# Optimization experiments

Hardware: AMD Instinct MI355X
Metric: run time of the kernel (lower is better)

The kernel has to match this reference:

```python
import jax, jax.numpy as jnp
import numpy as np

D_MODEL = 512
NHEAD = 8


def setup_inputs() -> dict:
    key = jax.random.key(0)
    k0, k1, k2 = jax.random.split(key, 3)
    s = 1.0 / np.sqrt(D_MODEL)  # torch default uniform init bound (xavier-ish)
    return {
        "x": jax.random.normal(k0, (2, 4096, D_MODEL), dtype=jnp.float32),
        "in_proj_w": jax.random.uniform(k1, (3 * D_MODEL, D_MODEL), jnp.float32, -s, s),
        "in_proj_b": jnp.zeros((3 * D_MODEL,), jnp.float32),
        "out_proj_w": jax.random.uniform(k2, (D_MODEL, D_MODEL), jnp.float32, -s, s),
        "out_proj_b": jnp.zeros((D_MODEL,), jnp.float32),
        "window_size": 128,
    }


def reference(x, in_proj_w, in_proj_b, out_proj_w, out_proj_b, window_size):
    # Faithful to nn.MultiheadAttention (eval mode, dropout inactive).
    # NOTE: PyTorch bool attn_mask: True = disallowed. The module sets True
    # INSIDE the window, so in-window positions are masked OUT.
    B, S, D = x.shape
    H = NHEAD
    hd = D // H

    qkv = x @ in_proj_w.T + in_proj_b                      # [B,S,3D]
    q, k, v = jnp.split(qkv, 3, axis=-1)
    q = q.reshape(B, S, H, hd).transpose(0, 2, 1, 3)       # [B,H,S,hd]
    k = k.reshape(B, S, H, hd).transpose(0, 2, 1, 3)
    v = v.reshape(B, S, H, hd).transpose(0, 2, 1, 3)

    scores = jnp.einsum('bhqd,bhkd->bhqk', q, k) / jnp.sqrt(jnp.float32(hd))

    idx = jnp.arange(S)
    in_window = jnp.abs(idx[:, None] - idx[None, :]) <= window_size  # [S,S]
    scores = jnp.where(in_window, -jnp.inf, scores)

    attn = jax.nn.softmax(scores, axis=-1)                 # [B,H,S,S]
    ctx = jnp.einsum('bhqk,bhkd->bhqd', attn, v)           # [B,H,S,hd]
    ctx = ctx.transpose(0, 2, 1, 3).reshape(B, S, D)       # [B,S,D]
    return ctx @ out_proj_w.T + out_proj_b
```

## Files before the change

kernel.cpp:

```cpp
#include <hip/hip_runtime.h>
#include <hip/hip_bf16.h>

typedef unsigned short u16;
typedef __bf16 bf16x8 __attribute__((ext_vector_type(8)));
typedef float f32x4 __attribute__((ext_vector_type(4)));

__device__ __forceinline__ f32x4 mfma16(bf16x8 a, bf16x8 b, f32x4 c) {
    return __builtin_amdgcn_mfma_f32_16x16x32_bf16(a, b, c, 0, 0, 0);
}

__device__ __forceinline__ u16 f2b(float x) {
    union { float f; unsigned u; } a; a.f = x;
    unsigned r = a.u + 0x7fffu + ((a.u >> 16) & 1u);
    return (u16)(r >> 16);
}

__global__ __launch_bounds__(256) void k_cast(const float* __restrict__ src,
                                              u16* __restrict__ dst, int n) {
    int i = (blockIdx.x * 256 + threadIdx.x) * 4;
    if (i >= n) return;
    float4 f = *(const float4*)&src[i];
    u16 o[4] = { f2b(f.x), f2b(f.y), f2b(f.z), f2b(f.w) };
    *(uint2*)&dst[i] = *(uint2*)o;
}

__global__ __launch_bounds__(256) void k_gemm_qkv(const u16* __restrict__ xb,
                                                  const u16* __restrict__ wb,
                                                  const float* __restrict__ bias,
                                                  u16* __restrict__ qkvout) {
    __shared__ u16 As[128][40];
    __shared__ u16 Ws[64][40];
    const int tid = threadIdx.x;
    const int w = tid >> 6, lane = tid & 63, l15 = lane & 15, quad = lane >> 4;
    const int mb = blockIdx.x * 128, nb = blockIdx.y * 64;

    f32x4 acc[2][4];
#pragma unroll
    for (int i = 0; i < 2; i++)
#pragma unroll
        for (int j = 0; j < 4; j++) acc[i][j] = (f32x4){0.f, 0.f, 0.f, 0.f};

    for (int k0 = 0; k0 < 512; k0 += 32) {
        {
            int row = tid >> 1, cc = (tid & 1) * 16;
            const u16* g = &xb[(size_t)(mb + row) * 512 + k0 + cc];
            *(uint4*)&As[row][cc]     = *(const uint4*)g;
            *(uint4*)&As[row][cc + 8] = *(const uint4*)(g + 8);
            int wrow = tid >> 2, wcc = (tid & 3) * 8;
            *(uint4*)&Ws[wrow][wcc] = *(const uint4*)&wb[(size_t)(nb + wrow) * 512 + k0 + wcc];
        }
        __syncthreads();
        bf16x8 a0 = *(const bf16x8*)&As[w * 32 + l15][quad * 8];
        bf16x8 a1 = *(const bf16x8*)&As[w * 32 + 16 + l15][quad * 8];
#pragma unroll
        for (int nt = 0; nt < 4; nt++) {
            bf16x8 bfr = *(const bf16x8*)&Ws[nt * 16 + l15][quad * 8];
            acc[0][nt] = mfma16(a0, bfr, acc[0][nt]);
            acc[1][nt] = mfma16(a1, bfr, acc[1][nt]);
        }
        __syncthreads();
    }
    const int seg = nb >> 9;
    const int hh  = (nb >> 6) & 7;
    u16* obase = qkvout + (size_t)seg * (16ull * 4096 * 64);
    if (seg < 2) {
        const float sc = (seg == 0) ? 0.125f * 1.44269504088896340736f : 1.0f;
#pragma unroll
        for (int mt = 0; mt < 2; mt++)
#pragma unroll
            for (int nt = 0; nt < 4; nt++)
#pragma unroll
                for (int r = 0; r < 4; r++) {
                    int m = mb + w * 32 + mt * 16 + quad * 4 + r;
                    int dloc = nt * 16 + l15;
                    float vv = (acc[mt][nt][r] + bias[nb + dloc]) * sc;
                    int b = m >> 12, s = m & 4095;
                    obase[((size_t)((b * 8 + hh) * 4096 + s)) * 64 + dloc] = f2b(vv);
                }
    } else {
#pragma unroll
        for (int mt = 0; mt < 2; mt++)
#pragma unroll
            for (int nt = 0; nt < 4; nt++) {
                int m0 = mb + w * 32 + mt * 16 + quad * 4;
                int b = m0 >> 12, s0 = m0 & 4095;
                int dloc = nt * 16 + l15;
                u16 o[4];
#pragma unroll
                for (int r = 0; r < 4; r++)
                    o[r] = f2b(acc[mt][nt][r] + bias[nb + dloc]);
                *(uint2*)&obase[((size_t)((b * 8 + hh) * 64 + dloc)) * 4096 + s0] = *(uint2*)o;
            }
    }
}

__global__ __launch_bounds__(128) void k_attn(const u16* __restrict__ qkv,
                                              u16* __restrict__ ctx,
                                              const int* __restrict__ win) {
    __shared__ u16 Ks[64][72];
    __shared__ u16 Vt[64][72];
    __shared__ u16 Ps[64][72];
    const int tid = threadIdx.x;
    const int w = tid >> 6, lane = tid & 63, l15 = lane & 15, quad = lane >> 4;
    const int bh = blockIdx.y;
    const int qb0 = blockIdx.x * 64;
    const int W = win[0];
    const u16* qg = qkv;
    const u16* kg = qkv + 16ull * 4096 * 64;
    const u16* vg = qkv + 32ull * 4096 * 64;
    const size_t bhb = (size_t)bh * 4096 * 64;

    bf16x8 qf[2][2];
#pragma unroll
    for (int g = 0; g < 2; g++) {
        const u16* qrow = &qg[bhb + (size_t)(qb0 + w * 32 + g * 16 + l15) * 64];
        qf[g][0] = *(const bf16x8*)&qrow[quad * 8];
        qf[g][1] = *(const bf16x8*)&qrow[32 + quad * 8];
    }

    f32x4 O[2][4];
#pragma unroll
    for (int g = 0; g < 2; g++)
#pragma unroll
        for (int nt = 0; nt < 4; nt++) O[g][nt] = (f32x4){0.f, 0.f, 0.f, 0.f};
    float lsum[2] = {0.f, 0.f};

    const int srow = tid >> 1, shalf = (tid & 1) * 32;
    const u16* kgr = &kg[bhb + (size_t)srow * 64 + shalf];
    const u16* vgr = &vg[((size_t)bh * 64 + srow) * 4096 + shalf];

    for (int kb = 0; kb < 4096; kb += 64) {
        if (max(qb0 + 63 - kb, kb + 63 - qb0) <= W) continue;
        bool partial = (kb + 63 >= qb0 - W) && (kb <= qb0 + 63 + W);
        {
            const u16* kp = kgr + (size_t)kb * 64;
            *(uint4*)&Ks[srow][shalf]      = *(const uint4*)kp;
            *(uint4*)&Ks[srow][shalf + 8]  = *(const uint4*)(kp + 8);
            *(uint4*)&Ks[srow][shalf + 16] = *(const uint4*)(kp + 16);
            *(uint4*)&Ks[srow][shalf + 24] = *(const uint4*)(kp + 24);
            const u16* vp = vgr + kb;
            *(uint4*)&Vt[srow][shalf]      = *(const uint4*)vp;
            *(uint4*)&Vt[srow][shalf + 8]  = *(const uint4*)(vp + 8);
            *(uint4*)&Vt[srow][shalf + 16] = *(const uint4*)(vp + 16);
            *(uint4*)&Vt[srow][shalf + 24] = *(const uint4*)(vp + 24);
        }
        __syncthreads();
        f32x4 C[4][2];
#pragma unroll
        for (int nt = 0; nt < 4; nt++) {
            bf16x8 kf0 = *(const bf16x8*)&Ks[nt * 16 + l15][quad * 8];
            bf16x8 kf1 = *(const bf16x8*)&Ks[nt * 16 + l15][32 + quad * 8];
#pragma unroll
            for (int g = 0; g < 2; g++) {
                f32x4 z = (f32x4){0.f, 0.f, 0.f, 0.f};
                C[nt][g] = mfma16(kf0, qf[g][0], z);
                C[nt][g] = mfma16(kf1, qf[g][1], C[nt][g]);
            }
        }
        if (!partial) {
#pragma unroll
            for (int g = 0; g < 2; g++)
#pragma unroll
                for (int nt = 0; nt < 4; nt++) {
                    u16 o[4];
#pragma unroll
                    for (int r = 0; r < 4; r++) {
                        float p = __builtin_amdgcn_exp2f(C[nt][g][r]);
                        lsum[g] += p;
                        o[r] = f2b(p);
                    }
                    *(uint2*)&Ps[w * 32 + g * 16 + l15][nt * 16 + quad * 4] = *(uint2*)o;
                }
        } else {
#pragma unroll
            for (int g = 0; g < 2; g++) {
                int qr = qb0 + w * 32 + g * 16 + l15;
#pragma unroll
                for (int nt = 0; nt < 4; nt++) {
                    u16 o[4];
#pragma unroll
                    for (int r = 0; r < 4; r++) {
                        int key = kb + nt * 16 + quad * 4 + r;
                        int dd = qr - key; dd = dd < 0 ? -dd : dd;
                        float p = (dd <= W) ? 0.f : __builtin_amdgcn_exp2f(C[nt][g][r]);
                        lsum[g] += p;
                        o[r] = f2b(p);
                    }
                    *(uint2*)&Ps[w * 32 + g * 16 + l15][nt * 16 + quad * 4] = *(uint2*)o;
                }
            }
        }
#pragma unroll
        for (int ks = 0; ks < 2; ks++) {
            bf16x8 pa0 = *(const bf16x8*)&Ps[w * 32 + l15][ks * 32 + quad * 8];
            bf16x8 pa1 = *(const bf16x8*)&Ps[w * 32 + 16 + l15][ks * 32 + quad * 8];
#pragma unroll
            for (int nt = 0; nt < 4; nt++) {
                bf16x8 vb = *(const bf16x8*)&Vt[nt * 16 + l15][ks * 32 + quad * 8];
                O[0][nt] = mfma16(pa0, vb, O[0][nt]);
                O[1][nt] = mfma16(pa1, vb, O[1][nt]);
            }
        }
        __syncthreads();
    }
#pragma unroll
    for (int g = 0; g < 2; g++) {
        lsum[g] += __shfl_xor(lsum[g], 16);
        lsum[g] += __shfl_xor(lsum[g], 32);
    }
    int b = bh >> 3, h = bh & 7;
#pragma unroll
    for (int g = 0; g < 2; g++)
#pragma unroll
        for (int r = 0; r < 4; r++) {
            float inv = 1.0f / __shfl(lsum[g], quad * 4 + r);
            int qr = qb0 + w * 32 + g * 16 + quad * 4 + r;
            size_t rowoff = ((size_t)(b * 4096 + qr)) * 512 + h * 64;
#pragma unroll
            for (int nt = 0; nt < 4; nt++)
                ctx[rowoff + nt * 16 + l15] = f2b(O[g][nt][r] * inv);
        }
}

__global__ __launch_bounds__(256) void k_gemm_out(const u16* __restrict__ ab,
                                                  const u16* __restrict__ wb,
                                                  const float* __restrict__ bias,
                                                  float* __restrict__ out) {
    __shared__ u16 As[128][40];
    __shared__ u16 Ws[64][40];
    const int tid = threadIdx.x;
    const int w = tid >> 6, lane = tid & 63, l15 = lane & 15, quad = lane >> 4;
    const int mb = blockIdx.x * 128, nb = blockIdx.y * 64;

    f32x4 acc[2][4];
#pragma unroll
    for (int i = 0; i < 2; i++)
#pragma unroll
        for (int j = 0; j < 4; j++) acc[i][j] = (f32x4){0.f, 0.f, 0.f, 0.f};

    for (int k0 = 0; k0 < 512; k0 += 32) {
        {
            int row = tid >> 1, cc = (tid & 1) * 16;
            const u16* g = &ab[(size_t)(mb + row) * 512 + k0 + cc];
            *(uint4*)&As[row][cc]     = *(const uint4*)g;
            *(uint4*)&As[row][cc + 8] = *(const uint4*)(g + 8);
            int wrow = tid >> 2, wcc = (tid & 3) * 8;
            *(uint4*)&Ws[wrow][wcc] = *(const uint4*)&wb[(size_t)(nb + wrow) * 512 + k0 + wcc];
        }
        __syncthreads();
        bf16x8 a0 = *(const bf16x8*)&As[w * 32 + l15][quad * 8];
        bf16x8 a1 = *(const bf16x8*)&As[w * 32 + 16 + l15][quad * 8];
#pragma unroll
        for (int nt = 0; nt < 4; nt++) {
            bf16x8 bfr = *(const bf16x8*)&Ws[nt * 16 + l15][quad * 8];
            acc[0][nt] = mfma16(a0, bfr, acc[0][nt]);
            acc[1][nt] = mfma16(a1, bfr, acc[1][nt]);
        }
        __syncthreads();
    }
#pragma unroll
    for (int mt = 0; mt < 2; mt++)
#pragma unroll
        for (int nt = 0; nt < 4; nt++)
#pragma unroll
            for (int r = 0; r < 4; r++) {
                int m = mb + w * 32 + mt * 16 + quad * 4 + r;
                int n = nb + nt * 16 + l15;
                out[(size_t)m * 512 + n] = acc[mt][nt][r] + bias[n];
            }
}

extern "C" void kernel_launch(void* const* d_in, const int* in_sizes, int n_in,
                              void* d_out, int out_size, void* d_ws, size_t ws_size,
                              hipStream_t stream) {
    const float* x    = (const float*)d_in[0];
    const float* wqkv = (const float*)d_in[1];
    const float* bqkv = (const float*)d_in[2];
    const float* wout = (const float*)d_in[3];
    const float* bout = (const float*)d_in[4];
    const int*   win  = (const int*)d_in[5];
    float* out = (float*)d_out;

    u16* xb    = (u16*)d_ws;
    u16* wqkvb = xb    + 8192ull * 512;
    u16* woutb = wqkvb + 1536ull * 512;
    u16* qkvb  = woutb + 512ull * 512;
    u16* ctxb  = qkvb  + 3ull * 16 * 4096 * 64;

    k_cast<<<4096, 256, 0, stream>>>(x, xb, 8192 * 512);
    k_cast<<<768, 256, 0, stream>>>(wqkv, wqkvb, 1536 * 512);
    k_cast<<<256, 256, 0, stream>>>(wout, woutb, 512 * 512);
    k_gemm_qkv<<<dim3(64, 24), 256, 0, stream>>>(xb, wqkvb, bqkv, qkvb);
    k_attn<<<dim3(64, 16), 128, 0, stream>>>(qkvb, ctxb, win);
    k_gemm_out<<<dim3(64, 8), 256, 0, stream>>>(ctxb, woutb, bout, out);
}
```

Before: 239.1 us.

## Fuse fp32-to-bf16 casts into GEMM loads and enlarge attention query tile

```diff
diff --git a/kernel.cpp b/kernel.cpp
--- a/kernel.cpp
+++ b/kernel.cpp
@@ -15,17 +15,8 @@
     return (u16)(r >> 16);
 }
 
-__global__ __launch_bounds__(256) void k_cast(const float* __restrict__ src,
-                                              u16* __restrict__ dst, int n) {
-    int i = (blockIdx.x * 256 + threadIdx.x) * 4;
-    if (i >= n) return;
-    float4 f = *(const float4*)&src[i];
-    u16 o[4] = { f2b(f.x), f2b(f.y), f2b(f.z), f2b(f.w) };
-    *(uint2*)&dst[i] = *(uint2*)o;
-}
-
-__global__ __launch_bounds__(256) void k_gemm_qkv(const u16* __restrict__ xb,
-                                                  const u16* __restrict__ wb,
+__global__ __launch_bounds__(256) void k_gemm_qkv(const float* __restrict__ x,
+                                                  const float* __restrict__ wqkv,
                                                   const float* __restrict__ bias,
                                                   u16* __restrict__ qkvout) {
     __shared__ u16 As[128][40];
@@ -42,12 +33,23 @@
 
     for (int k0 = 0; k0 < 512; k0 += 32) {
         {
-            int row = tid >> 1, cc = (tid & 1) * 16;
-            const u16* g = &xb[(size_t)(mb + row) * 512 + k0 + cc];
-            *(uint4*)&As[row][cc]     = *(const uint4*)g;
-            *(uint4*)&As[row][cc + 8] = *(const uint4*)(g + 8);
-            int wrow = tid >> 2, wcc = (tid & 3) * 8;
-            *(uint4*)&Ws[wrow][wcc] = *(const uint4*)&wb[(size_t)(nb + wrow) * 512 + k0 + wcc];
+            int row = tid >> 1, seg = (tid & 1) * 16;
+            const float* g = &x[(size_t)(mb + row) * 512 + k0 + seg];
+            u16 o[16];
+#pragma unroll
+            for (int e = 0; e < 4; e++) {
+                float4 f = *(const float4*)(g + e * 4);
+                o[e * 4 + 0] = f2b(f.x); o[e * 4 + 1] = f2b(f.y);
+                o[e * 4 + 2] = f2b(f.z); o[e * 4 + 3] = f2b(f.w);
+            }
+            *(uint4*)&As[row][seg]     = *(uint4*)&o[0];
+            *(uint4*)&As[row][seg + 8] = *(uint4*)&o[8];
+            int wrow = tid >> 2, wseg = (tid & 3) * 8;
+            const float* gw = &wqkv[(size_t)(nb + wrow) * 512 + k0 + wseg];
+            float4 h0 = *(const float4*)gw, h1 = *(const float4*)(gw + 4);
+            u16 ow[8] = { f2b(h0.x), f2b(h0.y), f2b(h0.z), f2b(h0.w),
+                          f2b(h1.x), f2b(h1.y), f2b(h1.z), f2b(h1.w) };
+            *(uint4*)&Ws[wrow][wseg] = *(uint4*)ow;
         }
         __syncthreads();
         bf16x8 a0 = *(const bf16x8*)&As[w * 32 + l15][quad * 8];
@@ -99,39 +101,39 @@
                                               const int* __restrict__ win) {
     __shared__ u16 Ks[64][72];
     __shared__ u16 Vt[64][72];
-    __shared__ u16 Ps[64][72];
+    __shared__ u16 Ps[128][72];
     const int tid = threadIdx.x;
     const int w = tid >> 6, lane = tid & 63, l15 = lane & 15, quad = lane >> 4;
     const int bh = blockIdx.y;
-    const int qb0 = blockIdx.x * 64;
+    const int qb0 = blockIdx.x * 128;
     const int W = win[0];
     const u16* qg = qkv;
     const u16* kg = qkv + 16ull * 4096 * 64;
     const u16* vg = qkv + 32ull * 4096 * 64;
     const size_t bhb = (size_t)bh * 4096 * 64;
 
-    bf16x8 qf[2][2];
-#pragma unroll
-    for (int g = 0; g < 2; g++) {
-        const u16* qrow = &qg[bhb + (size_t)(qb0 + w * 32 + g * 16 + l15) * 64];
+    bf16x8 qf[4][2];
+#pragma unroll
+    for (int g = 0; g < 4; g++) {
+        const u16* qrow = &qg[bhb + (size_t)(qb0 + w * 64 + g * 16 + l15) * 64];
         qf[g][0] = *(const bf16x8*)&qrow[quad * 8];
         qf[g][1] = *(const bf16x8*)&qrow[32 + quad * 8];
     }
 
-    f32x4 O[2][4];
-#pragma unroll
-    for (int g = 0; g < 2; g++)
+    f32x4 O[4][4];
+#pragma unroll
+    for (int g = 0; g < 4; g++)
 #pragma unroll
         for (int nt = 0; nt < 4; nt++) O[g][nt] = (f32x4){0.f, 0.f, 0.f, 0.f};
-    float lsum[2] = {0.f, 0.f};
+    float lsum[4] = {0.f, 0.f, 0.f, 0.f};
 
     const int srow = tid >> 1, shalf = (tid & 1) * 32;
     const u16* kgr = &kg[bhb + (size_t)srow * 64 + shalf];
     const u16* vgr = &vg[((size_t)bh * 64 + srow) * 4096 + shalf];
 
     for (int kb = 0; kb < 4096; kb += 64) {
-        if (max(qb0 + 63 - kb, kb + 63 - qb0) <= W) continue;
-        bool partial = (kb + 63 >= qb0 - W) && (kb <= qb0 + 63 + W);
+        if (max(qb0 + 127 - kb, kb + 63 - qb0) <= W) continue;
+        bool partial = (kb + 63 >= qb0 - W) && (kb <= qb0 + 127 + W);
         {
             const u16* kp = kgr + (size_t)kb * 64;
             *(uint4*)&Ks[srow][shalf]      = *(const uint4*)kp;
@@ -145,36 +147,35 @@
             *(uint4*)&Vt[srow][shalf + 24] = *(const uint4*)(vp + 24);
         }
         __syncthreads();
-        f32x4 C[4][2];
+        bf16x8 kf[4][2];
 #pragma unroll
         for (int nt = 0; nt < 4; nt++) {
-            bf16x8 kf0 = *(const bf16x8*)&Ks[nt * 16 + l15][quad * 8];
-            bf16x8 kf1 = *(const bf16x8*)&Ks[nt * 16 + l15][32 + quad * 8];
-#pragma unroll
-            for (int g = 0; g < 2; g++) {
+            kf[nt][0] = *(const bf16x8*)&Ks[nt * 16 + l15][quad * 8];
+            kf[nt][1] = *(const bf16x8*)&Ks[nt * 16 + l15][32 + quad * 8];
+        }
+#pragma unroll
+        for (int g = 0; g < 4; g++) {
+            f32x4 C[4];
+#pragma unroll
+            for (int nt = 0; nt < 4; nt++) {
                 f32x4 z = (f32x4){0.f, 0.f, 0.f, 0.f};
-                C[nt][g] = mfma16(kf0, qf[g][0], z);
-                C[nt][g] = mfma16(kf1, qf[g][1], C[nt][g]);
-            }
-        }
-        if (!partial) {
-#pragma unroll
-            for (int g = 0; g < 2; g++)
+                C[nt] = mfma16(kf[nt][0], qf[g][0], z);
+                C[nt] = mfma16(kf[nt][1], qf[g][1], C[nt]);
+            }
+            if (!partial) {
 #pragma unroll
                 for (int nt = 0; nt < 4; nt++) {
                     u16 o[4];
 #pragma unroll
                     for (int r = 0; r < 4; r++) {
-                        float p = __builtin_amdgcn_exp2f(C[nt][g][r]);
+                        float p = __builtin_amdgcn_exp2f(C[nt][r]);
                         lsum[g] += p;
                         o[r] = f2b(p);
                     }
-                    *(uint2*)&Ps[w * 32 + g * 16 + l15][nt * 16 + quad * 4] = *(uint2*)o;
+                    *(uint2*)&Ps[w * 64 + g * 16 + l15][nt * 16 + quad * 4] = *(uint2*)o;
                 }
-        } else {
-#pragma unroll
-            for (int g = 0; g < 2; g++) {
-                int qr = qb0 + w * 32 + g * 16 + l15;
+            } else {
+                int qr = qb0 + w * 64 + g * 16 + l15;
 #pragma unroll
                 for (int nt = 0; nt < 4; nt++) {
                     u16 o[4];
@@ -182,39 +183,42 @@
                     for (int r = 0; r < 4; r++) {
                         int key = kb + nt * 16 + quad * 4 + r;
                         int dd = qr - key; dd = dd < 0 ? -dd : dd;
-                        float p = (dd <= W) ? 0.f : __builtin_amdgcn_exp2f(C[nt][g][r]);
+                        float p = (dd <= W) ? 0.f : __builtin_amdgcn_exp2f(C[nt][r]);
                         lsum[g] += p;
                         o[r] = f2b(p);
                     }
-                    *(uint2*)&Ps[w * 32 + g * 16 + l15][nt * 16 + quad * 4] = *(uint2*)o;
+                    *(uint2*)&Ps[w * 64 + g * 16 + l15][nt * 16 + quad * 4] = *(uint2*)o;
                 }
             }
         }
 #pragma unroll
         for (int ks = 0; ks < 2; ks++) {
-            bf16x8 pa0 = *(const bf16x8*)&Ps[w * 32 + l15][ks * 32 + quad * 8];
-            bf16x8 pa1 = *(const bf16x8*)&Ps[w * 32 + 16 + l15][ks * 32 + quad * 8];
+            bf16x8 pa[4];
+#pragma unroll
+            for (int g = 0; g < 4; g++)
+                pa[g] = *(const bf16x8*)&Ps[w * 64 + g * 16 + l15][ks * 32 + quad * 8];
 #pragma unroll
             for (int nt = 0; nt < 4; nt++) {
                 bf16x8 vb = *(const bf16x8*)&Vt[nt * 16 + l15][ks * 32 + quad * 8];
-                O[0][nt] = mfma16(pa0, vb, O[0][nt]);
-                O[1][nt] = mfma16(pa1, vb, O[1][nt]);
-            }
-        }
-        __syncthreads();
-    }
-#pragma unroll
-    for (int g = 0; g < 2; g++) {
+#pragma unroll
+                for (int g = 0; g < 4; g++)
+                    O[g][nt] = mfma16(pa[g], vb, O[g][nt]);
+            }
+        }
+        __syncthreads();
+    }
+#pragma unroll
+    for (int g = 0; g < 4; g++) {
         lsum[g] += __shfl_xor(lsum[g], 16);
         lsum[g] += __shfl_xor(lsum[g], 32);
     }
     int b = bh >> 3, h = bh & 7;
 #pragma unroll
-    for (int g = 0; g < 2; g++)
+    for (int g = 0; g < 4; g++)
 #pragma unroll
         for (int r = 0; r < 4; r++) {
             float inv = 1.0f / __shfl(lsum[g], quad * 4 + r);
-            int qr = qb0 + w * 32 + g * 16 + quad * 4 + r;
+            int qr = qb0 + w * 64 + g * 16 + quad * 4 + r;
             size_t rowoff = ((size_t)(b * 4096 + qr)) * 512 + h * 64;
 #pragma unroll
             for (int nt = 0; nt < 4; nt++)
@@ -223,7 +227,7 @@
 }
 
 __global__ __launch_bounds__(256) void k_gemm_out(const u16* __restrict__ ab,
-                                                  const u16* __restrict__ wb,
+                                                  const float* __restrict__ wout,
                                                   const float* __restrict__ bias,
                                                   float* __restrict__ out) {
     __shared__ u16 As[128][40];
@@ -244,8 +248,12 @@
             const u16* g = &ab[(size_t)(mb + row) * 512 + k0 + cc];
             *(uint4*)&As[row][cc]     = *(const uint4*)g;
             *(uint4*)&As[row][cc + 8] = *(const uint4*)(g + 8);
-            int wrow = tid >> 2, wcc = (tid & 3) * 8;
-            *(uint4*)&Ws[wrow][wcc] = *(const uint4*)&wb[(size_t)(nb + wrow) * 512 + k0 + wcc];
+            int wrow = tid >> 2, wseg = (tid & 3) * 8;
+            const float* gw = &wout[(size_t)(nb + wrow) * 512 + k0 + wseg];
+            float4 h0 = *(const float4*)gw, h1 = *(const float4*)(gw + 4);
+            u16 ow[8] = { f2b(h0.x), f2b(h0.y), f2b(h0.z), f2b(h0.w),
+                          f2b(h1.x), f2b(h1.y), f2b(h1.z), f2b(h1.w) };
+            *(uint4*)&Ws[wrow][wseg] = *(uint4*)ow;
         }
         __syncthreads();
         bf16x8 a0 = *(const bf16x8*)&As[w * 32 + l15][quad * 8];
@@ -281,16 +289,10 @@
     const int*   win  = (const int*)d_in[5];
     float* out = (float*)d_out;
 
-    u16* xb    = (u16*)d_ws;
-    u16* wqkvb = xb    + 8192ull * 512;
-    u16* woutb = wqkvb + 1536ull * 512;
-    u16* qkvb  = woutb + 512ull * 512;
-    u16* ctxb  = qkvb  + 3ull * 16 * 4096 * 64;
-
-    k_cast<<<4096, 256, 0, stream>>>(x, xb, 8192 * 512);
-    k_cast<<<768, 256, 0, stream>>>(wqkv, wqkvb, 1536 * 512);
-    k_cast<<<256, 256, 0, stream>>>(wout, woutb, 512 * 512);
-    k_gemm_qkv<<<dim3(64, 24), 256, 0, stream>>>(xb, wqkvb, bqkv, qkvb);
-    k_attn<<<dim3(64, 16), 128, 0, stream>>>(qkvb, ctxb, win);
-    k_gemm_out<<<dim3(64, 8), 256, 0, stream>>>(ctxb, woutb, bout, out);
-}
+    u16* qkvb = (u16*)d_ws;
+    u16* ctxb = qkvb + 3ull * 16 * 4096 * 64;
+
+    k_gemm_qkv<<<dim3(64, 24), 256, 0, stream>>>(x, wqkv, bqkv, qkvb);
+    k_attn<<<dim3(32, 16), 128, 0, stream>>>(qkvb, ctxb, win);
+    k_gemm_out<<<dim3(64, 8), 256, 0, stream>>>(ctxb, wout, bout, out);
+}
```

Measured after the change: 301.0 us. +25.9%, slower.

## Keep attention probabilities in registers and widen GEMM N-tiles to 128

Applied to the files above, without the earlier changes.

```diff
diff --git a/kernel.cpp b/kernel.cpp
--- a/kernel.cpp
+++ b/kernel.cpp
@@ -3,10 +3,14 @@
 
 typedef unsigned short u16;
 typedef __bf16 bf16x8 __attribute__((ext_vector_type(8)));
+typedef short s16x4 __attribute__((ext_vector_type(4)));
 typedef float f32x4 __attribute__((ext_vector_type(4)));
 
 __device__ __forceinline__ f32x4 mfma16(bf16x8 a, bf16x8 b, f32x4 c) {
     return __builtin_amdgcn_mfma_f32_16x16x32_bf16(a, b, c, 0, 0, 0);
+}
+__device__ __forceinline__ f32x4 mfma16k16(s16x4 a, s16x4 b, f32x4 c) {
+    return __builtin_amdgcn_mfma_f32_16x16x16bf16_1k(a, b, c, 0, 0, 0);
 }
 
 __device__ __forceinline__ u16 f2b(float x) {
@@ -29,16 +33,16 @@
                                                   const float* __restrict__ bias,
                                                   u16* __restrict__ qkvout) {
     __shared__ u16 As[128][40];
-    __shared__ u16 Ws[64][40];
+    __shared__ u16 Ws[128][40];
     const int tid = threadIdx.x;
     const int w = tid >> 6, lane = tid & 63, l15 = lane & 15, quad = lane >> 4;
-    const int mb = blockIdx.x * 128, nb = blockIdx.y * 64;
-
-    f32x4 acc[2][4];
+    const int mb = blockIdx.x * 128, nb = blockIdx.y * 128;
+
+    f32x4 acc[2][8];
 #pragma unroll
     for (int i = 0; i < 2; i++)
 #pragma unroll
-        for (int j = 0; j < 4; j++) acc[i][j] = (f32x4){0.f, 0.f, 0.f, 0.f};
+        for (int j = 0; j < 8; j++) acc[i][j] = (f32x4){0.f, 0.f, 0.f, 0.f};
 
     for (int k0 = 0; k0 < 512; k0 += 32) {
         {
@@ -46,14 +50,15 @@
             const u16* g = &xb[(size_t)(mb + row) * 512 + k0 + cc];
             *(uint4*)&As[row][cc]     = *(const uint4*)g;
             *(uint4*)&As[row][cc + 8] = *(const uint4*)(g + 8);
-            int wrow = tid >> 2, wcc = (tid & 3) * 8;
-            *(uint4*)&Ws[wrow][wcc] = *(const uint4*)&wb[(size_t)(nb + wrow) * 512 + k0 + wcc];
+            const u16* gw = &wb[(size_t)(nb + row) * 512 + k0 + cc];
+            *(uint4*)&Ws[row][cc]     = *(const uint4*)gw;
+            *(uint4*)&Ws[row][cc + 8] = *(const uint4*)(gw + 8);
         }
         __syncthreads();
         bf16x8 a0 = *(const bf16x8*)&As[w * 32 + l15][quad * 8];
         bf16x8 a1 = *(const bf16x8*)&As[w * 32 + 16 + l15][quad * 8];
 #pragma unroll
-        for (int nt = 0; nt < 4; nt++) {
+        for (int nt = 0; nt < 8; nt++) {
             bf16x8 bfr = *(const bf16x8*)&Ws[nt * 16 + l15][quad * 8];
             acc[0][nt] = mfma16(a0, bfr, acc[0][nt]);
             acc[1][nt] = mfma16(a1, bfr, acc[1][nt]);
@@ -61,45 +66,47 @@
         __syncthreads();
     }
     const int seg = nb >> 9;
-    const int hh  = (nb >> 6) & 7;
     u16* obase = qkvout + (size_t)seg * (16ull * 4096 * 64);
     if (seg < 2) {
         const float sc = (seg == 0) ? 0.125f * 1.44269504088896340736f : 1.0f;
 #pragma unroll
         for (int mt = 0; mt < 2; mt++)
 #pragma unroll
-            for (int nt = 0; nt < 4; nt++)
+            for (int nt = 0; nt < 8; nt++) {
+                int dcol = nb + nt * 16 + l15;
+                int hh = (dcol >> 6) & 7, dloc = dcol & 63;
+                float bs = bias[dcol];
 #pragma unroll
                 for (int r = 0; r < 4; r++) {
                     int m = mb + w * 32 + mt * 16 + quad * 4 + r;
-                    int dloc = nt * 16 + l15;
-                    float vv = (acc[mt][nt][r] + bias[nb + dloc]) * sc;
+                    float vv = (acc[mt][nt][r] + bs) * sc;
                     int b = m >> 12, s = m & 4095;
                     obase[((size_t)((b * 8 + hh) * 4096 + s)) * 64 + dloc] = f2b(vv);
                 }
+            }
     } else {
 #pragma unroll
         for (int mt = 0; mt < 2; mt++)
 #pragma unroll
-            for (int nt = 0; nt < 4; nt++) {
+            for (int nt = 0; nt < 8; nt++) {
+                int dcol = nb + nt * 16 + l15;
+                int hh = (dcol >> 6) & 7, dloc = dcol & 63;
+                float bs = bias[dcol];
                 int m0 = mb + w * 32 + mt * 16 + quad * 4;
                 int b = m0 >> 12, s0 = m0 & 4095;
-                int dloc = nt * 16 + l15;
                 u16 o[4];
 #pragma unroll
-                for (int r = 0; r < 4; r++)
-                    o[r] = f2b(acc[mt][nt][r] + bias[nb + dloc]);
+                for (int r = 0; r < 4; r++) o[r] = f2b(acc[mt][nt][r] + bs);
                 *(uint2*)&obase[((size_t)((b * 8 + hh) * 64 + dloc)) * 4096 + s0] = *(uint2*)o;
             }
     }
 }
 
-__global__ __launch_bounds__(128) void k_attn(const u16* __restrict__ qkv,
-                                              u16* __restrict__ ctx,
-                                              const int* __restrict__ win) {
+__global__ __launch_bounds__(128, 2) void k_attn(const u16* __restrict__ qkv,
+                                                 u16* __restrict__ ctx,
+                                                 const int* __restrict__ win) {
     __shared__ u16 Ks[64][72];
     __shared__ u16 Vt[64][72];
-    __shared__ u16 Ps[64][72];
     const int tid = threadIdx.x;
     const int w = tid >> 6, lane = tid & 63, l15 = lane & 15, quad = lane >> 4;
     const int bh = blockIdx.y;
@@ -122,7 +129,7 @@
 #pragma unroll
     for (int g = 0; g < 2; g++)
 #pragma unroll
-        for (int nt = 0; nt < 4; nt++) O[g][nt] = (f32x4){0.f, 0.f, 0.f, 0.f};
+        for (int mb = 0; mb < 4; mb++) O[g][mb] = (f32x4){0.f, 0.f, 0.f, 0.f};
     float lsum[2] = {0.f, 0.f};
 
     const int srow = tid >> 1, shalf = (tid & 1) * 32;
@@ -145,61 +152,55 @@
             *(uint4*)&Vt[srow][shalf + 24] = *(const uint4*)(vp + 24);
         }
         __syncthreads();
-        f32x4 C[4][2];
+        bf16x8 kf[4][2];
 #pragma unroll
         for (int nt = 0; nt < 4; nt++) {
-            bf16x8 kf0 = *(const bf16x8*)&Ks[nt * 16 + l15][quad * 8];
-            bf16x8 kf1 = *(const bf16x8*)&Ks[nt * 16 + l15][32 + quad * 8];
-#pragma unroll
-            for (int g = 0; g < 2; g++) {
+            kf[nt][0] = *(const bf16x8*)&Ks[nt * 16 + l15][quad * 8];
+            kf[nt][1] = *(const bf16x8*)&Ks[nt * 16 + l15][32 + quad * 8];
+        }
+        s16x4 vf[4][4];
+#pragma unroll
+        for (int mb = 0; mb < 4; mb++)
+#pragma unroll
+            for (int nt = 0; nt < 4; nt++)
+                vf[mb][nt] = *(const s16x4*)&Vt[mb * 16 + l15][nt * 16 + quad * 4];
+#pragma unroll
+        for (int g = 0; g < 2; g++) {
+            f32x4 C[4];
+#pragma unroll
+            for (int nt = 0; nt < 4; nt++) {
                 f32x4 z = (f32x4){0.f, 0.f, 0.f, 0.f};
-                C[nt][g] = mfma16(kf0, qf[g][0], z);
-                C[nt][g] = mfma16(kf1, qf[g][1], C[nt][g]);
-            }
-        }
-        if (!partial) {
-#pragma unroll
-            for (int g = 0; g < 2; g++)
-#pragma unroll
-                for (int nt = 0; nt < 4; nt++) {
-                    u16 o[4];
+                C[nt] = mfma16(kf[nt][0], qf[g][0], z);
+                C[nt] = mfma16(kf[nt][1], qf[g][1], C[nt]);
+            }
+            s16x4 pb[4];
+            if (!partial) {
+#pragma unroll
+                for (int nt = 0; nt < 4; nt++)
 #pragma unroll
                     for (int r = 0; r < 4; r++) {
-                        float p = __builtin_amdgcn_exp2f(C[nt][g][r]);
+                        float p = __builtin_amdgcn_exp2f(C[nt][r]);
                         lsum[g] += p;
-                        o[r] = f2b(p);
+                        pb[nt][r] = (short)f2b(p);
                     }
-                    *(uint2*)&Ps[w * 32 + g * 16 + l15][nt * 16 + quad * 4] = *(uint2*)o;
-                }
-        } else {
-#pragma unroll
-            for (int g = 0; g < 2; g++) {
+            } else {
                 int qr = qb0 + w * 32 + g * 16 + l15;
 #pragma unroll
-                for (int nt = 0; nt < 4; nt++) {
-                    u16 o[4];
+                for (int nt = 0; nt < 4; nt++)
 #pragma unroll
                     for (int r = 0; r < 4; r++) {
                         int key = kb + nt * 16 + quad * 4 + r;
                         int dd = qr - key; dd = dd < 0 ? -dd : dd;
-                        float p = (dd <= W) ? 0.f : __builtin_amdgcn_exp2f(C[nt][g][r]);
+                        float p = (dd <= W) ? 0.f : __builtin_amdgcn_exp2f(C[nt][r]);
                         lsum[g] += p;
-                        o[r] = f2b(p);
+                        pb[nt][r] = (short)f2b(p);
                     }
-                    *(uint2*)&Ps[w * 32 + g * 16 + l15][nt * 16 + quad * 4] = *(uint2*)o;
-                }
-            }
-        }
-#pragma unroll
-        for (int ks = 0; ks < 2; ks++) {
-            bf16x8 pa0 = *(const bf16x8*)&Ps[w * 32 + l15][ks * 32 + quad * 8];
-            bf16x8 pa1 = *(const bf16x8*)&Ps[w * 32 + 16 + l15][ks * 32 + quad * 8];
-#pragma unroll
-            for (int nt = 0; nt < 4; nt++) {
-                bf16x8 vb = *(const bf16x8*)&Vt[nt * 16 + l15][ks * 32 + quad * 8];
-                O[0][nt] = mfma16(pa0, vb, O[0][nt]);
-                O[1][nt] = mfma16(pa1, vb, O[1][nt]);
-            }
+            }
+#pragma unroll
+            for (int nt = 0; nt < 4; nt++)
+#pragma unroll
+                for (int mb = 0; mb < 4; mb++)
+                    O[g][mb] = mfma16k16(vf[mb][nt], pb[nt], O[g][mb]);
         }
         __syncthreads();
     }
@@ -210,16 +211,18 @@
     }
     int b = bh >> 3, h = bh & 7;
 #pragma unroll
-    for (int g = 0; g < 2; g++)
-#pragma unroll
-        for (int r = 0; r < 4; r++) {
-            float inv = 1.0f / __shfl(lsum[g], quad * 4 + r);
-            int qr = qb0 + w * 32 + g * 16 + quad * 4 + r;
-            size_t rowoff = ((size_t)(b * 4096 + qr)) * 512 + h * 64;
-#pragma unroll
-            for (int nt = 0; nt < 4; nt++)
-                ctx[rowoff + nt * 16 + l15] = f2b(O[g][nt][r] * inv);
-        }
+    for (int g = 0; g < 2; g++) {
+        float inv = 1.0f / lsum[g];
+        int qr = qb0 + w * 32 + g * 16 + l15;
+        size_t rowoff = ((size_t)(b * 4096 + qr)) * 512 + h * 64;
+#pragma unroll
+        for (int mb = 0; mb < 4; mb++) {
+            u16 o[4];
+#pragma unroll
+            for (int r = 0; r < 4; r++) o[r] = f2b(O[g][mb][r] * inv);
+            *(uint2*)&ctx[rowoff + mb * 16 + quad * 4] = *(uint2*)o;
+        }
+    }
 }
 
 __global__ __launch_bounds__(256) void k_gemm_out(const u16* __restrict__ ab,
@@ -227,16 +230,16 @@
                                                   const float* __restrict__ bias,
                                                   float* __restrict__ out) {
     __shared__ u16 As[128][40];
-    __shared__ u16 Ws[64][40];
+    __shared__ u16 Ws[128][40];
     const int tid = threadIdx.x;
     const int w = tid >> 6, lane = tid & 63, l15 = lane & 15, quad = lane >> 4;
-    const int mb = blockIdx.x * 128, nb = blockIdx.y * 64;
-
-    f32x4 acc[2][4];
+    const int mb = blockIdx.x * 128, nb = blockIdx.y * 128;
+
+    f32x4 acc[2][8];
 #pragma unroll
     for (int i = 0; i < 2; i++)
 #pragma unroll
-        for (int j = 0; j < 4; j++) acc[i][j] = (f32x4){0.f, 0.f, 0.f, 0.f};
+        for (int j = 0; j < 8; j++) acc[i][j] = (f32x4){0.f, 0.f, 0.f, 0.f};
 
     for (int k0 = 0; k0 < 512; k0 += 32) {
         {
@@ -244,14 +247,15 @@
             const u16* g = &ab[(size_t)(mb + row) * 512 + k0 + cc];
             *(uint4*)&As[row][cc]     = *(const uint4*)g;
             *(uint4*)&As[row][cc + 8] = *(const uint4*)(g + 8);
-            int wrow = tid >> 2, wcc = (tid & 3) * 8;
-            *(uint4*)&Ws[wrow][wcc] = *(const uint4*)&wb[(size_t)(nb + wrow) * 512 + k0 + wcc];
+            const u16* gw = &wb[(size_t)(nb + row) * 512 + k0 + cc];
+            *(uint4*)&Ws[row][cc]     = *(const uint4*)gw;
+            *(uint4*)&Ws[row][cc + 8] = *(const uint4*)(gw + 8);
         }
         __syncthreads();
         bf16x8 a0 = *(const bf16x8*)&As[w * 32 + l15][quad * 8];
         bf16x8 a1 = *(const bf16x8*)&As[w * 32 + 16 + l15][quad * 8];
 #pragma unroll
-        for (int nt = 0; nt < 4; nt++) {
+        for (int nt = 0; nt < 8; nt++) {
             bf16x8 bfr = *(const bf16x8*)&Ws[nt * 16 + l15][quad * 8];
             acc[0][nt] = mfma16(a0, bfr, acc[0][nt]);
             acc[1][nt] = mfma16(a1, bfr, acc[1][nt]);
@@ -261,13 +265,15 @@
 #pragma unroll
     for (int mt = 0; mt < 2; mt++)
 #pragma unroll
-        for (int nt = 0; nt < 4; nt++)
+        for (int nt = 0; nt < 8; nt++) {
+            int n = nb + nt * 16 + l15;
+            float bs = bias[n];
 #pragma unroll
             for (int r = 0; r < 4; r++) {
                 int m = mb + w * 32 + mt * 16 + quad * 4 + r;
-                int n = nb + nt * 16 + l15;
-                out[(size_t)m * 512 + n] = acc[mt][nt][r] + bias[n];
-            }
+                out[(size_t)m * 512 + n] = acc[mt][nt][r] + bs;
+            }
+        }
 }
 
 extern "C" void kernel_launch(void* const* d_in, const int* in_sizes, int n_in,
@@ -290,7 +296,7 @@
     k_cast<<<4096, 256, 0, stream>>>(x, xb, 8192 * 512);
     k_cast<<<768, 256, 0, stream>>>(wqkv, wqkvb, 1536 * 512);
     k_cast<<<256, 256, 0, stream>>>(wout, woutb, 512 * 512);
-    k_gemm_qkv<<<dim3(64, 24), 256, 0, stream>>>(xb, wqkvb, bqkv, qkvb);
+    k_gemm_qkv<<<dim3(64, 12), 256, 0, stream>>>(xb, wqkvb, bqkv, qkvb);
     k_attn<<<dim3(64, 16), 128, 0, stream>>>(qkvb, ctxb, win);
-    k_gemm_out<<<dim3(64, 8), 256, 0, stream>>>(ctxb, woutb, bout, out);
-}
+    k_gemm_out<<<dim3(64, 4), 256, 0, stream>>>(ctxb, woutb, bout, out);
+}
```

Measured after the change: 240.2 us. About the same (+0.5%).
